# Kernel optimization log

Measured on AMD Instinct MI355X. Metric: run time of the kernel, lower is better.

The kernel has to match this reference:

```python
import jax, jax.numpy as jnp
import numpy as np

B, T, C, H = 2, 2048, 1024, 16
HS = C // H        # head dim = 64
HALF = HS // 2     # rope half = 32


def _rope_cos_sin():
    # standard RoPE frequencies over the half-dim
    inv_freq = 1.0 / (10000.0 ** (np.arange(HALF, dtype=np.float32) / HALF))
    t = np.arange(T, dtype=np.float32)
    ang = np.outer(t, inv_freq)  # [T, HALF]
    cos = np.cos(ang)[None, None]  # [1,1,T,HALF]
    sin = np.sin(ang)[None, None]
    return jnp.asarray(cos), jnp.asarray(sin)


def setup_inputs() -> dict:
    key = jax.random.key(0)
    k1, k2, k3 = jax.random.split(key, 3)
    cos, sin = _rope_cos_sin()
    return {
        "x": jax.random.normal(k1, (B, T, C), dtype=jnp.float32),
        "cos": cos,
        "sin": sin,
        "w_attn": jax.random.normal(k2, (C, 3 * C), dtype=jnp.float32) * (1.0 / np.sqrt(C)),
        "b_attn": jnp.zeros((3 * C,), dtype=jnp.float32),
        "w_proj": jax.random.normal(k3, (C, C), dtype=jnp.float32) * (1.0 / np.sqrt(C)),
        "b_proj": jnp.zeros((C,), dtype=jnp.float32),
    }


def _rope_apply(x, cos, sin):
    # x: [B,H,T,HS]; cos/sin: [1,1,T,HALF]
    x1, x2 = x[..., :HALF], x[..., HALF:]
    return jnp.concatenate([x1 * cos - x2 * sin, x1 * sin + x2 * cos], axis=-1)


def reference(x, cos, sin, w_attn, b_attn, w_proj, b_proj):
    b, t, c = x.shape
    qkv = x @ w_attn + b_attn                      # [B,T,3C]
    q, k, v = jnp.split(qkv, 3, axis=-1)
    # [B,T,C] -> [B,H,T,HS]
    def to_heads(u):
        return u.reshape(b, t, H, HS).transpose(0, 2, 1, 3)
    q, k, v = to_heads(q), to_heads(k), to_heads(v)
    q = _rope_apply(q, cos[:, :, :t], sin[:, :, :t])
    k = _rope_apply(k, cos[:, :, :t], sin[:, :, :t])
    scale = 1.0 / np.sqrt(HS).astype(np.float32)
    scores = jnp.einsum("bhqd,bhkd->bhqk", q, k) * scale
    causal = jnp.tril(jnp.ones((t, t), dtype=bool))
    scores = jnp.where(causal, scores, jnp.finfo(scores.dtype).min)
    attn = jax.nn.softmax(scores, axis=-1)
    ctx = jnp.einsum("bhqk,bhkd->bhqd", attn, v)   # [B,H,T,HS]
    ctx = ctx.transpose(0, 2, 1, 3).reshape(b, t, c)
    return ctx @ w_proj + b_proj
```

## Files before the change

### kernel.cpp

```cpp
#include <hip/hip_runtime.h>
#include <hip/hip_bf16.h>

#define Bn    2
#define Tdim  2048
#define Cdim  1024
#define Hn    16
#define HSd   64
#define Mrows 4096

typedef unsigned short u16;
typedef __attribute__((ext_vector_type(8))) short short8;
typedef __attribute__((ext_vector_type(4))) float f32x4;

__device__ __forceinline__ u16 f2bf(float f) {
  union { __hip_bfloat16 h; u16 u; } cv;
  cv.h = __float2bfloat16(f);
  return cv.u;
}

#define GLOAD_LDS16(g, l)                                                     \
  __builtin_amdgcn_global_load_lds(                                           \
      (const __attribute__((address_space(1))) void*)(g),                     \
      (__attribute__((address_space(3))) void*)(l), 16, 0, 0)

#define CFENCE asm volatile("" ::: "memory")

__global__ __launch_bounds__(256) void k_prep(const float* __restrict__ x,
                                              u16* __restrict__ xb,
                                              const float* __restrict__ wattn,
                                              u16* __restrict__ wattnT,
                                              const float* __restrict__ wproj,
                                              u16* __restrict__ wprojT) {
  __shared__ float tile[64][65];
  const int bid = blockIdx.x, tid = threadIdx.x;
  if (bid < 4096) {
    int i = bid * 256 + tid;
    float4 v = ((const float4*)x)[i];
    unsigned o0 = (unsigned)f2bf(v.x) | ((unsigned)f2bf(v.y) << 16);
    unsigned o1 = (unsigned)f2bf(v.z) | ((unsigned)f2bf(v.w) << 16);
    ((uint2*)xb)[i] = make_uint2(o0, o1);
    return;
  }
  const float* in;
  u16* out;
  int Cc, c0, r0;
  if (bid < 4096 + 768) {
    int b = bid - 4096;
    in = wattn; out = wattnT; Cc = 3072;
    c0 = (b % 48) * 64; r0 = (b / 48) * 64;
  } else {
    int b = bid - 4864;
    in = wproj; out = wprojT; Cc = 1024;
    c0 = (b % 16) * 64; r0 = (b / 16) * 64;
  }
  const int R = 1024;
  int lc = tid & 63, l0 = tid >> 6;
  for (int rr = l0; rr < 64; rr += 4)
    tile[rr][lc] = in[(size_t)(r0 + rr) * Cc + c0 + lc];
  __syncthreads();
  for (int rr = l0; rr < 64; rr += 4)
    out[(size_t)(c0 + rr) * R + r0 + lc] = f2bf(tile[lc][rr]);
}

__global__ __launch_bounds__(256) void k_transpose_v(const u16* __restrict__ Vh,
                                                     u16* __restrict__ Vt) {
  __shared__ u16 tile[64][72];
  int bh = blockIdx.y, t0 = blockIdx.x * 64;
  int lc = threadIdx.x & 63, l0 = threadIdx.x >> 6;
  const u16* src = Vh + (size_t)bh * Tdim * HSd;
  u16* dst = Vt + (size_t)bh * HSd * Tdim;
  for (int rr = l0; rr < 64; rr += 4)
    tile[rr][lc] = src[(size_t)(t0 + rr) * HSd + lc];
  __syncthreads();
  for (int dd = l0; dd < 64; dd += 4)
    dst[(size_t)dd * Tdim + t0 + lc] = tile[lc][dd];
}

template <int EPI, int BM, int BN, int WM, int WN, int MINW>
__global__ __launch_bounds__(64 * WM * WN, MINW) void k_gemm2(
    const u16* __restrict__ A, const u16* __restrict__ Bt,
    const float* __restrict__ bias, const float* __restrict__ cosT,
    const float* __restrict__ sinT, u16* __restrict__ Qh, u16* __restrict__ Kh,
    u16* __restrict__ Vh, float* __restrict__ Out, int Ndim, int Kdim) {
  __shared__ u16 As[3][BM * 32];
  __shared__ u16 Bs[3][BN * 32];
  u16* const Asm = &As[0][0];
  u16* const Bsm = &Bs[0][0];
  const int tid = threadIdx.x;
  const int wid = tid >> 6, lane = tid & 63;
  const int wr = wid / WN, wc = wid % WN;
  const int lr = lane & 15, lg = lane >> 4;
  const int m0 = blockIdx.x * BM, n0 = blockIdx.y * BN;
  const int wm = wr * 64, wn = wc * 64;

  f32x4 acc[4][4] = {};

  const u16* Ag = A + (size_t)m0 * Kdim;
  const u16* Bg = Bt + (size_t)n0 * Kdim;
  const int srw = lane >> 2;
  const int scb = ((lane & 3) ^ ((lane >> 3) & 3)) << 4;
  constexpr int NW = WM * WN;
  constexpr int CPW = (BM + BN) / 16 / NW;
  constexpr int CA = BM / 16;
  static_assert(CPW == 3 || CPW == 4, "vmcnt literal table");

#define STAGE2(bi, t)                                                         \
  do {                                                                        \
    u16* aDst = Asm + (bi) * (BM * 32);                                       \
    u16* bDst = Bsm + (bi) * (BN * 32);                                       \
    _Pragma("unroll") for (int cc = 0; cc < CPW; ++cc) {                      \
      int c = wid * CPW + cc;                                                 \
      if (c < CA)                                                             \
        GLOAD_LDS16(                                                          \
            (const char*)(Ag + (size_t)(c * 16 + srw) * Kdim + (t)*32) + scb, \
            aDst + c * 512);                                                  \
      else                                                                    \
        GLOAD_LDS16((const char*)(Bg + (size_t)((c - CA) * 16 + srw) * Kdim + \
                                  (t)*32) +                                   \
                        scb,                                                  \
                    bDst + (c - CA) * 512);                                   \
    }                                                                         \
  } while (0)

#define WAIT_CPW                                                              \
  do {                                                                        \
    if constexpr (CPW == 3)                                                   \
      asm volatile("s_waitcnt vmcnt(3)" ::: "memory");                        \
    else                                                                      \
      asm volatile("s_waitcnt vmcnt(4)" ::: "memory");                        \
  } while (0)

#define LDFRAG(buf, row)                                                      \
  (*(const short8*)((const char*)(buf) + (row)*64 +                           \
                    ((lg * 16) ^ ((((row) >> 1) & 3) << 4))))

  const int nt = Kdim >> 5;
  STAGE2(0, 0);
  STAGE2(1, 1);
  WAIT_CPW;
  __builtin_amdgcn_s_barrier();
  CFENCE;

  int cur = 0;
  for (int t = 0; t < nt; ++t) {
    int st = cur + 2;
    if (st >= 3) st -= 3;
    if (t + 2 < nt) STAGE2(st, t + 2);
    CFENCE;
    const u16* ab = Asm + cur * (BM * 32);
    const u16* bb = Bsm + cur * (BN * 32);
    short8 a[4], b[4];
#pragma unroll
    for (int i = 0; i < 4; ++i) a[i] = LDFRAG(ab, wm + i * 16 + lr);
#pragma unroll
    for (int j = 0; j < 4; ++j) b[j] = LDFRAG(bb, wn + j * 16 + lr);
    __builtin_amdgcn_s_setprio(1);
#pragma unroll
    for (int i = 0; i < 4; ++i)
#pragma unroll
      for (int j = 0; j < 4; ++j)
        acc[i][j] =
            __builtin_amdgcn_mfma_f32_16x16x32_bf16(a[i], b[j], acc[i][j], 0, 0, 0);
    __builtin_amdgcn_s_setprio(0);
    CFENCE;
    if (t + 2 < nt)
      WAIT_CPW;
    else if (t + 2 == nt)
      asm volatile("s_waitcnt vmcnt(0)" ::: "memory");
    if (t + 1 < nt) {
      __builtin_amdgcn_s_barrier();
      CFENCE;
    }
    cur = (cur == 2) ? 0 : cur + 1;
  }
#undef STAGE2
#undef WAIT_CPW
#undef LDFRAG

  const int nbase = n0 + wn;
  if (EPI == 0) {
    const int sec = nbase >> 10;
    const int hh = (nbase & 1023) >> 6;
    const float qs = (sec == 0) ? 0.125f : 1.0f;
    float bj[4];
#pragma unroll
    for (int nj = 0; nj < 4; ++nj) bj[nj] = bias[nbase + nj * 16 + lr];
#pragma unroll
    for (int mi = 0; mi < 4; ++mi) {
      int growb = m0 + wm + mi * 16 + 4 * lg;
#pragma unroll
      for (int r = 0; r < 4; ++r) {
        int gr = growb + r;
        int bI = gr >> 11, tq = gr & (Tdim - 1);
        size_t off = ((size_t)(bI * Hn + hh) * Tdim + tq) * HSd;
        if (sec < 2) {
          u16* dst = (sec == 0) ? Qh : Kh;
#pragma unroll
          for (int nj = 0; nj < 2; ++nj) {
            int d = nj * 16 + lr;
            float v1 = acc[mi][nj][r] + bj[nj];
            float v2 = acc[mi][nj + 2][r] + bj[nj + 2];
            float cs = cosT[tq * 32 + d], sn = sinT[tq * 32 + d];
            dst[off + d] = f2bf((v1 * cs - v2 * sn) * qs);
            dst[off + d + 32] = f2bf((v1 * sn + v2 * cs) * qs);
          }
        } else {
#pragma unroll
          for (int nj = 0; nj < 4; ++nj)
            Vh[off + nj * 16 + lr] = f2bf(acc[mi][nj][r] + bj[nj]);
        }
      }
    }
  } else {
#pragma unroll
    for (int mi = 0; mi < 4; ++mi) {
      int growb = m0 + wm + mi * 16 + 4 * lg;
#pragma unroll
      for (int r = 0; r < 4; ++r) {
        int gr = growb + r;
#pragma unroll
        for (int nj = 0; nj < 4; ++nj) {
          int col = nbase + nj * 16 + lr;
          Out[(size_t)gr * Ndim + col] = acc[mi][nj][r] + bias[col];
        }
      }
    }
  }
}

__global__ __launch_bounds__(512, 4) void k_attn(const u16* __restrict__ Qh,
                                                 const u16* __restrict__ Kh,
                                                 const u16* __restrict__ Vt,
                                                 u16* __restrict__ ctx) {
  __shared__ u16 Ks[2][64 * 64];
  __shared__ u16 Vs[2][64 * 64];
  __shared__ u16 Plds[8][16][72];
  const int tid = threadIdx.x;
  const int wid = tid >> 6, lane = tid & 63;
  const int lr = lane & 15, lg = lane >> 4;
  const int bid = blockIdx.x;
  const int xb = 15 - (bid >> 5);
  const int bh = bid & 31;
  const int qr0 = xb * 128 + wid * 16;
  const int nt = 2 * xb + 2;
  const int itd = qr0 >> 6;
  const u16* Q = Qh + (size_t)bh * Tdim * HSd;
  const u16* K = Kh + (size_t)bh * Tdim * HSd;
  const u16* V = Vt + (size_t)bh * HSd * Tdim;

  short8 qf0 = *(const short8*)(Q + (size_t)(qr0 + lr) * HSd + 8 * lg);
  short8 qf1 = *(const short8*)(Q + (size_t)(qr0 + lr) * HSd + 32 + 8 * lg);

  const int srow = lane >> 3;
  const int scol = 16 * ((lane & 7) ^ srow);
  const int swz = (lr & 7) << 4;

  f32x4 ctxa[4] = {};
  float ssum[4] = {0.f, 0.f, 0.f, 0.f};
  const float L2E = 1.44269504089f;
  const float MC = 24.0f * L2E;
  const f32x4 zero = {};

#define STAGE_KV(b, kv0)                                                      \
  do {                                                                        \
    GLOAD_LDS16((const char*)(K + (size_t)((kv0) + wid * 8 + srow) * HSd) +   \
                    scol,                                                     \
                Ks[b] + wid * 8 * 64);                                        \
    GLOAD_LDS16((const char*)(V + (size_t)(wid * 8 + srow) * Tdim + (kv0)) +  \
                    scol,                                                     \
                Vs[b] + wid * 8 * 64);                                        \
  } while (0)

  STAGE_KV(0, 0);
  __syncthreads();

  int cur = 0;
  for (int it = 0; it < nt; ++it) {
    const int kv0 = it * 64;
    if (it + 1 < nt) STAGE_KV(cur ^ 1, kv0 + 64);

    if (it <= itd) {
      const char* ksb = (const char*)(Ks[cur]);
      const char* vsb = (const char*)(Vs[cur]);

      f32x4 s[4];
#pragma unroll
      for (int f = 0; f < 4; ++f) {
        int row = 16 * f + lr;
        int c0 = (lg * 16) ^ swz;
        short8 kf0 = *(const short8*)(ksb + row * 128 + c0);
        short8 kf1 = *(const short8*)(ksb + row * 128 + (c0 ^ 64));
        s[f] = __builtin_amdgcn_mfma_f32_16x16x32_bf16(qf0, kf0, zero, 0, 0, 0);
        s[f] = __builtin_amdgcn_mfma_f32_16x16x32_bf16(qf1, kf1, s[f], 0, 0, 0);
      }

#pragma unroll
      for (int r = 0; r < 4; ++r) {
        if (it == itd) {
          int q = qr0 + 4 * lg + r;
#pragma unroll
          for (int f = 0; f < 4; ++f)
            if (kv0 + 16 * f + lr > q) s[f][r] = -1e30f;
        }
#pragma unroll
        for (int f = 0; f < 4; ++f) {
          float p = __builtin_amdgcn_exp2f(fmaf(s[f][r], L2E, -MC));
          ssum[r] += p;
          Plds[wid][4 * lg + r][16 * f + lr] = f2bf(p);
        }
      }

      const char* pb = (const char*)(&Plds[wid][0][0]);
      short8 pa0 = *(const short8*)(pb + lr * 144 + lg * 16);
      short8 pa1 = *(const short8*)(pb + lr * 144 + 64 + lg * 16);

#pragma unroll
      for (int dt = 0; dt < 4; ++dt) {
        int row = 16 * dt + lr;
        int c0 = (lg * 16) ^ swz;
        short8 vb0 = *(const short8*)(vsb + row * 128 + c0);
        short8 vb1 = *(const short8*)(vsb + row * 128 + (c0 ^ 64));
        ctxa[dt] =
            __builtin_amdgcn_mfma_f32_16x16x32_bf16(pa0, vb0, ctxa[dt], 0, 0, 0);
        ctxa[dt] =
            __builtin_amdgcn_mfma_f32_16x16x32_bf16(pa1, vb1, ctxa[dt], 0, 0, 0);
      }
    }

    __syncthreads();
    cur ^= 1;
  }
#undef STAGE_KV

  const int bI = bh >> 4, hh = bh & 15;
#pragma unroll
  for (int r = 0; r < 4; ++r) {
    float s = ssum[r];
    s += __shfl_xor(s, 1);
    s += __shfl_xor(s, 2);
    s += __shfl_xor(s, 4);
    s += __shfl_xor(s, 8);
    float inv = 1.0f / s;
    int t = qr0 + 4 * lg + r;
    size_t off = ((size_t)bI * Tdim + t) * Cdim + hh * HSd;
#pragma unroll
    for (int dt = 0; dt < 4; dt++)
      ctx[off + dt * 16 + lr] = f2bf(ctxa[dt][r] * inv);
  }
}

extern "C" void kernel_launch(void* const* d_in, const int* in_sizes, int n_in,
                              void* d_out, int out_size, void* d_ws,
                              size_t ws_size, hipStream_t stream) {
  const float* x = (const float*)d_in[0];
  const float* cosT = (const float*)d_in[1];
  const float* sinT = (const float*)d_in[2];
  const float* wattn = (const float*)d_in[3];
  const float* battn = (const float*)d_in[4];
  const float* wproj = (const float*)d_in[5];
  const float* bproj = (const float*)d_in[6];
  float* out = (float*)d_out;
  char* ws = (char*)d_ws;
  const size_t MB = 1024 * 1024;
  u16* xb = (u16*)(ws + 0);
  u16* Vt = (u16*)(ws + 0);
  u16* wattnT = (u16*)(ws + 8 * MB);
  u16* wprojT = (u16*)(ws + 14 * MB);
  u16* Qh = (u16*)(ws + 16 * MB);
  u16* Kh = (u16*)(ws + 24 * MB);
  u16* Vh = (u16*)(ws + 32 * MB);
  u16* ctx = (u16*)(ws + 40 * MB);

  k_prep<<<5120, 256, 0, stream>>>(x, xb, wattn, wattnT, wproj, wprojT);
  k_gemm2<0, 128, 256, 2, 4, 4><<<dim3(32, 12), 512, 0, stream>>>(
      xb, wattnT, battn, cosT, sinT, Qh, Kh, Vh, nullptr, 3072, 1024);
  k_transpose_v<<<dim3(32, 32), 256, 0, stream>>>(Vh, Vt);
  k_attn<<<512, 512, 0, stream>>>(Qh, Kh, Vt, ctx);
  k_gemm2<1, 128, 128, 2, 2, 3><<<dim3(32, 8), 256, 0, stream>>>(
      ctx, wprojT, bproj, nullptr, nullptr, nullptr, nullptr, nullptr, out,
      1024, 1024);
}
```

Measured before the change: 202.2 us.

## Triple-buffer K/V tiles and pass P through registers instead of LDS

```diff
diff --git a/kernel.cpp b/kernel.cpp
--- a/kernel.cpp
+++ b/kernel.cpp
@@ -232,9 +232,8 @@
                                                  const u16* __restrict__ Kh,
                                                  const u16* __restrict__ Vt,
                                                  u16* __restrict__ ctx) {
-  __shared__ u16 Ks[2][64 * 64];
-  __shared__ u16 Vs[2][64 * 64];
-  __shared__ u16 Plds[8][16][72];
+  __shared__ u16 Ks[3][64 * 64];
+  __shared__ u16 Vs[3][64 * 64];
   const int tid = threadIdx.x;
   const int wid = tid >> 6, lane = tid & 63;
   const int lr = lane & 15, lg = lane >> 4;
@@ -254,9 +253,12 @@
   const int srow = lane >> 3;
   const int scol = 16 * ((lane & 7) ^ srow);
   const int swz = (lr & 7) << 4;
+  const int vperm = ((((lg & 1) << 1) | (lg >> 1)) << 4);
+  const bool odd = (lg & 1) != 0;
+  const int f0i = (lg & 1) << 1;
 
   f32x4 ctxa[4] = {};
-  float ssum[4] = {0.f, 0.f, 0.f, 0.f};
+  float ssum = 0.f;
   const float L2E = 1.44269504089f;
   const float MC = 24.0f * L2E;
   const f32x4 zero = {};
@@ -272,75 +274,107 @@
   } while (0)
 
   STAGE_KV(0, 0);
-  __syncthreads();
+  STAGE_KV(1, 64);
+  asm volatile("s_waitcnt vmcnt(2)" ::: "memory");
+  __builtin_amdgcn_s_barrier();
+  CFENCE;
 
   int cur = 0;
   for (int it = 0; it < nt; ++it) {
     const int kv0 = it * 64;
-    if (it + 1 < nt) STAGE_KV(cur ^ 1, kv0 + 64);
+    int st = cur + 2;
+    if (st >= 3) st -= 3;
+    if (it + 2 < nt) STAGE_KV(st, kv0 + 128);
+    CFENCE;
 
     if (it <= itd) {
       const char* ksb = (const char*)(Ks[cur]);
       const char* vsb = (const char*)(Vs[cur]);
 
-      f32x4 s[4];
+      f32x4 sT[4];
 #pragma unroll
       for (int f = 0; f < 4; ++f) {
         int row = 16 * f + lr;
         int c0 = (lg * 16) ^ swz;
         short8 kf0 = *(const short8*)(ksb + row * 128 + c0);
         short8 kf1 = *(const short8*)(ksb + row * 128 + (c0 ^ 64));
-        s[f] = __builtin_amdgcn_mfma_f32_16x16x32_bf16(qf0, kf0, zero, 0, 0, 0);
-        s[f] = __builtin_amdgcn_mfma_f32_16x16x32_bf16(qf1, kf1, s[f], 0, 0, 0);
+        sT[f] = __builtin_amdgcn_mfma_f32_16x16x32_bf16(kf0, qf0, zero, 0, 0, 0);
+        sT[f] = __builtin_amdgcn_mfma_f32_16x16x32_bf16(kf1, qf1, sT[f], 0, 0, 0);
       }
 
-#pragma unroll
-      for (int r = 0; r < 4; ++r) {
-        if (it == itd) {
-          int q = qr0 + 4 * lg + r;
-#pragma unroll
-          for (int f = 0; f < 4; ++f)
-            if (kv0 + 16 * f + lr > q) s[f][r] = -1e30f;
+      float p[4][4];
+#pragma unroll
+      for (int f = 0; f < 4; ++f)
+#pragma unroll
+        for (int r = 0; r < 4; ++r) {
+          float sv = sT[f][r];
+          if (it == itd) {
+            if (kv0 + 16 * f + 4 * lg + r > qr0 + lr) sv = -1e30f;
+          }
+          float pv = __builtin_amdgcn_exp2f(fmaf(sv, L2E, -MC));
+          ssum += pv;
+          p[f][r] = pv;
         }
-#pragma unroll
-        for (int f = 0; f < 4; ++f) {
-          float p = __builtin_amdgcn_exp2f(fmaf(s[f][r], L2E, -MC));
-          ssum[r] += p;
-          Plds[wid][4 * lg + r][16 * f + lr] = f2bf(p);
-        }
+
+      unsigned pk[8], pp[8];
+#pragma unroll
+      for (int f = 0; f < 4; ++f) {
+        asm("v_cvt_pk_bf16_f32 %0, %1, %2"
+            : "=v"(pk[2 * f])
+            : "v"(p[f][0]), "v"(p[f][1]));
+        asm("v_cvt_pk_bf16_f32 %0, %1, %2"
+            : "=v"(pk[2 * f + 1])
+            : "v"(p[f][2]), "v"(p[f][3]));
       }
-
-      const char* pb = (const char*)(&Plds[wid][0][0]);
-      short8 pa0 = *(const short8*)(pb + lr * 144 + lg * 16);
-      short8 pa1 = *(const short8*)(pb + lr * 144 + 64 + lg * 16);
+#pragma unroll
+      for (int i = 0; i < 8; ++i)
+        pp[i] = (unsigned)__shfl_xor((int)pk[i], 16);
+
+      union U8 { unsigned u[4]; short8 s; };
+      U8 A0, A1;
+      A0.u[0] = odd ? pp[f0i] : pk[f0i];
+      A0.u[1] = odd ? pp[f0i + 1] : pk[f0i + 1];
+      A0.u[2] = odd ? pk[f0i] : pp[f0i];
+      A0.u[3] = odd ? pk[f0i + 1] : pp[f0i + 1];
+      A1.u[0] = odd ? pp[4 + f0i] : pk[4 + f0i];
+      A1.u[1] = odd ? pp[4 + f0i + 1] : pk[4 + f0i + 1];
+      A1.u[2] = odd ? pk[4 + f0i] : pp[4 + f0i];
+      A1.u[3] = odd ? pk[4 + f0i + 1] : pp[4 + f0i + 1];
 
 #pragma unroll
       for (int dt = 0; dt < 4; ++dt) {
         int row = 16 * dt + lr;
-        int c0 = (lg * 16) ^ swz;
+        int c0 = vperm ^ swz;
         short8 vb0 = *(const short8*)(vsb + row * 128 + c0);
         short8 vb1 = *(const short8*)(vsb + row * 128 + (c0 ^ 64));
         ctxa[dt] =
-            __builtin_amdgcn_mfma_f32_16x16x32_bf16(pa0, vb0, ctxa[dt], 0, 0, 0);
+            __builtin_amdgcn_mfma_f32_16x16x32_bf16(A0.s, vb0, ctxa[dt], 0, 0, 0);
         ctxa[dt] =
-            __builtin_amdgcn_mfma_f32_16x16x32_bf16(pa1, vb1, ctxa[dt], 0, 0, 0);
+            __builtin_amdgcn_mfma_f32_16x16x32_bf16(A1.s, vb1, ctxa[dt], 0, 0, 0);
       }
     }
 
-    __syncthreads();
-    cur ^= 1;
+    CFENCE;
+    if (it + 2 < nt)
+      asm volatile("s_waitcnt vmcnt(2)" ::: "memory");
+    else if (it + 1 < nt)
+      asm volatile("s_waitcnt vmcnt(0)" ::: "memory");
+    if (it + 1 < nt) {
+      __builtin_amdgcn_s_barrier();
+      CFENCE;
+    }
+    cur = (cur == 2) ? 0 : cur + 1;
   }
 #undef STAGE_KV
 
+  float sAll = ssum;
+  sAll += __shfl_xor(sAll, 16);
+  sAll += __shfl_xor(sAll, 32);
+
   const int bI = bh >> 4, hh = bh & 15;
 #pragma unroll
   for (int r = 0; r < 4; ++r) {
-    float s = ssum[r];
-    s += __shfl_xor(s, 1);
-    s += __shfl_xor(s, 2);
-    s += __shfl_xor(s, 4);
-    s += __shfl_xor(s, 8);
-    float inv = 1.0f / s;
+    float inv = 1.0f / __shfl(sAll, 4 * lg + r);
     int t = qr0 + 4 * lg + r;
     size_t off = ((size_t)bI * Tdim + t) * Cdim + hh * HSd;
 #pragma unroll
```

After: 211.2 us. +4.4%, slower.
